# Kernel optimization log

Hardware: AMD Instinct MI355X
Metric: run time of the kernel (lower is better)

The kernel has to match this reference:

```python
import jax, jax.numpy as jnp
import numpy as np
import math

B, T, D = 2, 2048, 1024
H = 16
DH = D // H
DFF = 4096
EPS = 1e-5


def setup_inputs() -> dict:
    key = jax.random.key(0)
    ks = jax.random.split(key, 10)
    x = jax.random.normal(ks[0], (B, T, D), dtype=jnp.float32)
    # bool mask, True above diagonal => masked (matches masked_fill semantics)
    causal_mask = jnp.triu(jnp.ones((T, T), dtype=bool), k=1)
    s = 0.02
    return {
        "x": x,
        "causal_mask": causal_mask,
        "gamma1": jnp.ones((D,), jnp.float32),
        "beta1": jnp.zeros((D,), jnp.float32),
        "wq": jax.random.normal(ks[1], (D, D), jnp.float32) * s,
        "wk": jax.random.normal(ks[2], (D, D), jnp.float32) * s,
        "wv": jax.random.normal(ks[3], (D, D), jnp.float32) * s,
        "wo": jax.random.normal(ks[4], (D, D), jnp.float32) * s,
        "gamma2": jnp.ones((D,), jnp.float32),
        "beta2": jnp.zeros((D,), jnp.float32),
        "w1": jax.random.normal(ks[5], (D, DFF), jnp.float32) * s,
        "b1": jnp.zeros((DFF,), jnp.float32),
        "w2": jax.random.normal(ks[6], (DFF, D), jnp.float32) * s,
        "b2": jnp.zeros((D,), jnp.float32),
    }


def _layer_norm(x, gamma, beta):
    mean = jnp.mean(x, axis=-1, keepdims=True)
    var = jnp.mean((x - mean) ** 2, axis=-1, keepdims=True)
    xhat = (x - mean) / jnp.sqrt(var + EPS)
    return gamma * xhat + beta


def _split_heads(x):
    b, t, d = x.shape
    return x.reshape(b, t, H, DH).transpose(0, 2, 1, 3)  # (B,H,T,Dh)


def reference(x, causal_mask, gamma1, beta1, wq, wk, wv, wo,
              gamma2, beta2, w1, b1, w2, b2):
    # --- attention sublayer (pre-LN) ---
    h = _layer_norm(x, gamma1, beta1)
    q = _split_heads(h @ wq)
    k = _split_heads(h @ wk)
    v = _split_heads(h @ wv)
    scores = jnp.einsum('bhqd,bhkd->bhqk', q, k) / math.sqrt(DH)  # (B,H,T,T)
    scores = jnp.where(causal_mask[None, None, :, :], -jnp.inf, scores)
    attn = jax.nn.softmax(scores, axis=-1)
    out = jnp.einsum('bhqk,bhkd->bhqd', attn, v)
    out = out.transpose(0, 2, 1, 3).reshape(x.shape)  # merge heads
    attn_out = out @ wo
    x = x + attn_out
    # --- FFN sublayer (pre-LN) ---
    h = _layer_norm(x, gamma2, beta2)
    ffn = jax.nn.gelu(h @ w1 + b1, approximate=False) @ w2 + b2
    return x + ffn
```

## Files before the change

### kernel.cpp

```cpp
#include <hip/hip_runtime.h>
#include <hip/hip_bf16.h>
#include <math.h>

#define B_   2
#define T_   2048
#define D_   1024
#define H_   16
#define DH_  64
#define DFF_ 4096
#define NTOK (B_*T_)

typedef __attribute__((ext_vector_type(8))) short short8;
typedef __attribute__((ext_vector_type(4))) float f32x4;

static __device__ __forceinline__ short f2bf(float f) {
    union { __hip_bfloat16 h; short s; } u;
    u.h = __float2bfloat16(f);
    return u.s;
}

static __device__ __forceinline__ f32x4 mfma16(short8 a, short8 b, f32x4 c) {
    return __builtin_amdgcn_mfma_f32_16x16x32_bf16(a, b, c, 0, 0, 0);
}

static __device__ __forceinline__ void gload16(const void* g, void* l) {
    __builtin_amdgcn_global_load_lds(
        (__attribute__((address_space(1))) void*)g,
        (__attribute__((address_space(3))) void*)l, 16, 0, 0);
}

static __device__ __forceinline__ short8 lds_read_sw(const short* base, int row, int kbyte) {
    const int off = (row << 7) + (kbyte ^ ((row & 7) << 4));
    return *reinterpret_cast<const short8*>(reinterpret_cast<const char*>(base) + off);
}

__global__ __launch_bounds__(256) void transpose_cast(
    const float* __restrict__ src, short* __restrict__ dst, int K, int N, float scale)
{
    __shared__ short tile[32][33];
    const int k0 = blockIdx.y * 32, n0 = blockIdx.x * 32;
    const int tx = threadIdx.x, ty = threadIdx.y;
    #pragma unroll
    for (int j = 0; j < 4; ++j) {
        int k = ty + j * 8;
        tile[k][tx] = f2bf(src[(size_t)(k0 + k) * N + n0 + tx] * scale);
    }
    __syncthreads();
    #pragma unroll
    for (int j = 0; j < 4; ++j) {
        int n = ty + j * 8;
        dst[(size_t)(n0 + n) * K + k0 + tx] = tile[tx][n];
    }
}

__global__ __launch_bounds__(256) void ln_kernel(
    const float* __restrict__ in, const float* __restrict__ gamma,
    const float* __restrict__ beta, short* __restrict__ out)
{
    const int row = blockIdx.x;
    const int t = threadIdx.x;
    const float4 v = *reinterpret_cast<const float4*>(in + (size_t)row * D_ + t * 4);
    float s  = v.x + v.y + v.z + v.w;
    float sq = v.x*v.x + v.y*v.y + v.z*v.z + v.w*v.w;
    #pragma unroll
    for (int off = 32; off >= 1; off >>= 1) {
        s  += __shfl_xor(s, off);
        sq += __shfl_xor(sq, off);
    }
    __shared__ float ps[4], pq[4];
    if ((t & 63) == 0) { ps[t >> 6] = s; pq[t >> 6] = sq; }
    __syncthreads();
    s  = ps[0] + ps[1] + ps[2] + ps[3];
    sq = pq[0] + pq[1] + pq[2] + pq[3];
    const float mean = s * (1.0f / D_);
    float var = sq * (1.0f / D_) - mean * mean;
    var = fmaxf(var, 0.0f);
    const float rstd = rsqrtf(var + 1e-5f);
    const float4 g = *reinterpret_cast<const float4*>(gamma + t * 4);
    const float4 b = *reinterpret_cast<const float4*>(beta  + t * 4);
    short4 o;
    o.x = f2bf(g.x * ((v.x - mean) * rstd) + b.x);
    o.y = f2bf(g.y * ((v.y - mean) * rstd) + b.y);
    o.z = f2bf(g.z * ((v.z - mean) * rstd) + b.z);
    o.w = f2bf(g.w * ((v.w - mean) * rstd) + b.w);
    *reinterpret_cast<short4*>(out + (size_t)row * D_ + t * 4) = o;
}

template<int BM, int BN, int EPI>
__global__ __launch_bounds__(512) void gemm_kernel(
    const short* __restrict__ A, const short* __restrict__ Bt,
    void* __restrict__ Cout, const float* __restrict__ resid,
    const float* __restrict__ bias, short* __restrict__ vaux,
    int M, int N, int K, int nbx)
{
    constexpr int MB = BM / 4 / 16;
    constexpr int NB = BN / 2 / 16;
    constexpr int JA = BM / 64;
    constexpr int JB = BN / 64;
    constexpr int J  = JA + JB;
    __shared__ short As[2][BM * 64];
    __shared__ short Bs[2][BN * 64];
    const int t = threadIdx.x;
    const int wid = t >> 6, lane = t & 63;
    const int lr = lane & 15, lk = lane >> 4;
    const int cpx = (int)gridDim.x >> 3;
    const int bid = (int)blockIdx.x;
    const int swz = (bid & 7) * cpx + (bid >> 3);
    const int m0 = (swz / nbx) * BM, n0 = (swz % nbx) * BN;
    const int wrow = (wid >> 1) * (BM / 4);
    const int wcol = (wid & 1) * (BN / 2);

    const char* aSrc[JA];
    const char* bSrc[JB];
    #pragma unroll
    for (int j = 0; j < JA; ++j) {
        const int off = j * 8192 + t * 16;
        const int r   = off >> 7;
        const int cb  = (off & 127) ^ ((r & 7) << 4);
        aSrc[j] = (const char*)(A + (size_t)(m0 + r) * K) + cb;
    }
    #pragma unroll
    for (int j = 0; j < JB; ++j) {
        const int off = j * 8192 + t * 16;
        const int r   = off >> 7;
        const int cb  = (off & 127) ^ ((r & 7) << 4);
        bSrc[j] = (const char*)(Bt + (size_t)(n0 + r) * K) + cb;
    }

    f32x4 acc[MB][NB];
    #pragma unroll
    for (int m = 0; m < MB; ++m)
        #pragma unroll
        for (int n = 0; n < NB; ++n) acc[m][n] = (f32x4){0.f, 0.f, 0.f, 0.f};

    const int NT = K >> 6;

    auto stage = [&](int bufsel, int ktile) {
        const int kb = ktile << 7;
        #pragma unroll
        for (int j = 0; j < JA; ++j)
            gload16(aSrc[j] + kb, (char*)As[bufsel] + j * 8192 + wid * 1024);
        #pragma unroll
        for (int j = 0; j < JB; ++j)
            gload16(bSrc[j] + kb, (char*)Bs[bufsel] + j * 8192 + wid * 1024);
    };
    auto compute = [&](int bufsel) {
        #pragma unroll
        for (int kk = 0; kk < 64; kk += 32) {
            short8 af[MB], bf[NB];
            #pragma unroll
            for (int m = 0; m < MB; ++m)
                af[m] = lds_read_sw(As[bufsel], wrow + m * 16 + lr, (kk + lk * 8) * 2);
            #pragma unroll
            for (int n = 0; n < NB; ++n)
                bf[n] = lds_read_sw(Bs[bufsel], wcol + n * 16 + lr, (kk + lk * 8) * 2);
            #pragma unroll
            for (int m = 0; m < MB; ++m)
                #pragma unroll
                for (int n = 0; n < NB; ++n)
                    acc[m][n] = mfma16(af[m], bf[n], acc[m][n]);
        }
    };

    stage(0, 0);
    stage(1, 1);

    for (int kt = 0; kt < NT - 1; ++kt) {
        asm volatile("s_waitcnt vmcnt(%0)" :: "n"(J) : "memory");
        __builtin_amdgcn_s_barrier();
        compute(kt & 1);
        __builtin_amdgcn_s_barrier();
        if (kt + 2 < NT) stage(kt & 1, kt + 2);
    }
    asm volatile("s_waitcnt vmcnt(0)" ::: "memory");
    __builtin_amdgcn_s_barrier();
    compute((NT - 1) & 1);

    #pragma unroll
    for (int m = 0; m < MB; ++m) {
        #pragma unroll
        for (int n = 0; n < NB; ++n) {
            #pragma unroll
            for (int r = 0; r < 4; ++r) {
                const int gr = m0 + wrow + m * 16 + lk * 4 + r;
                const int gc = n0 + wcol + n * 16 + lr;
                const size_t idx = (size_t)gr * N + gc;
                const float v = acc[m][n][r];
                if constexpr (EPI == 0) {
                    ((short*)Cout)[idx] = f2bf(v);
                } else if constexpr (EPI == 1) {
                    ((float*)Cout)[idx] = resid[idx] + v;
                } else if constexpr (EPI == 2) {
                    const float tt = v + bias[gc];
                    const float ge = 0.5f * tt * (1.0f + erff(tt * 0.70710678118654752f));
                    ((short*)Cout)[idx] = f2bf(ge);
                } else if constexpr (EPI == 3) {
                    ((float*)Cout)[idx] = resid[idx] + v + bias[gc];
                } else {
                    if (gc < 2048) {
                        ((short*)Cout)[idx] = f2bf(v);
                    } else {
                        const int hh = (gc - 2048) >> 6, dh = (gc - 2048) & 63;
                        const int bb = gr >> 11, tl = gr & 2047;
                        vaux[((size_t)((bb << 4) + hh) * 64 + dh) * 2048 + tl] = f2bf(v);
                    }
                }
            }
        }
    }
}

static __device__ __forceinline__ void attn_tile(
    const short* Kcur, const short* Vcur, char* pw,
    short8 qf0, short8 qf1, int q0, int kvb, bool diag,
    int lr, int lk, f32x4 (&o)[4], float (&mr)[4], float (&ls)[4])
{
    f32x4 s[4];
    #pragma unroll
    for (int n = 0; n < 4; ++n) s[n] = (f32x4){0.f, 0.f, 0.f, 0.f};
    #pragma unroll
    for (int n = 0; n < 4; ++n) {
        s[n] = mfma16(qf0, lds_read_sw(Kcur, n * 16 + lr, (lk * 8) * 2), s[n]);
        s[n] = mfma16(qf1, lds_read_sw(Kcur, n * 16 + lr, (32 + lk * 8) * 2), s[n]);
    }
    #pragma unroll
    for (int r = 0; r < 4; ++r) {
        const int qg = q0 + lk * 4 + r;
        float v0 = s[0][r], v1 = s[1][r], v2 = s[2][r], v3 = s[3][r];
        if (diag) {
            if (kvb +      lr > qg) v0 = -INFINITY;
            if (kvb + 16 + lr > qg) v1 = -INFINITY;
            if (kvb + 32 + lr > qg) v2 = -INFINITY;
            if (kvb + 48 + lr > qg) v3 = -INFINITY;
        }
        const float mxl = fmaxf(fmaxf(v0, v1), fmaxf(v2, v3));
        if (!__all(mxl <= mr[r] + 8.0f)) {
            float mx = mxl;
            mx = fmaxf(mx, __shfl_xor(mx, 1));
            mx = fmaxf(mx, __shfl_xor(mx, 2));
            mx = fmaxf(mx, __shfl_xor(mx, 4));
            mx = fmaxf(mx, __shfl_xor(mx, 8));
            const float mnew = fmaxf(mr[r], mx);
            const float alpha = __builtin_amdgcn_exp2f(mr[r] - mnew);
            o[0][r] *= alpha; o[1][r] *= alpha; o[2][r] *= alpha; o[3][r] *= alpha;
            ls[r] *= alpha;
            mr[r] = mnew;
        }
        const float p0 = __builtin_amdgcn_exp2f(v0 - mr[r]);
        const float p1 = __builtin_amdgcn_exp2f(v1 - mr[r]);
        const float p2 = __builtin_amdgcn_exp2f(v2 - mr[r]);
        const float p3 = __builtin_amdgcn_exp2f(v3 - mr[r]);
        ls[r] += p0 + p1 + p2 + p3;
        const int prow = lk * 4 + r;
        const int sw = (prow & 7) << 4;
        char* prb = pw + prow * 128;
        *(short*)(prb + (((     lr * 2)) ^ sw)) = f2bf(p0);
        *(short*)(prb + ((32 + lr * 2) ^ sw)) = f2bf(p1);
        *(short*)(prb + ((64 + lr * 2) ^ sw)) = f2bf(p2);
        *(short*)(prb + ((96 + lr * 2) ^ sw)) = f2bf(p3);
    }
    asm volatile("s_waitcnt lgkmcnt(0)" ::: "memory");
    #pragma unroll
    for (int kk = 0; kk < 2; ++kk) {
        const short8 pf = *reinterpret_cast<const short8*>(
            pw + lr * 128 + ((kk * 64 + lk * 16) ^ ((lr & 7) << 4)));
        #pragma unroll
        for (int n = 0; n < 4; ++n)
            o[n] = mfma16(pf, lds_read_sw((const short*)Vcur, n * 16 + lr, (kk * 32 + lk * 8) * 2), o[n]);
    }
}

__global__ __launch_bounds__(256) void attn_kernel(
    const short* __restrict__ qkv, const short* __restrict__ vT,
    short* __restrict__ attn)
{
    __shared__ short Ks[2][4096];
    __shared__ short Vs[2][4096];
    __shared__ short Ps[2][4][1024];
    const int xx = blockIdx.x;
    const int bh = blockIdx.y;
    const int qA = xx, qB = 31 - xx;
    const int b = bh >> 4, h = bh & 15;
    const int t = threadIdx.x;
    const int wid = t >> 6, lane = t & 63;
    const int lr = lane & 15, lk = lane >> 4;
    const int q0A = qA * 64 + wid * 16;
    const int q0B = qB * 64 + wid * 16;

    const short* qrowA = qkv + (size_t)(b * T_ + q0A + lr) * 3072 + h * 64;
    const short8 qfA0 = *reinterpret_cast<const short8*>(qrowA + lk * 8);
    const short8 qfA1 = *reinterpret_cast<const short8*>(qrowA + 32 + lk * 8);
    const short* qrowB = qkv + (size_t)(b * T_ + q0B + lr) * 3072 + h * 64;
    const short8 qfB0 = *reinterpret_cast<const short8*>(qrowB + lk * 8);
    const short8 qfB1 = *reinterpret_cast<const short8*>(qrowB + 32 + lk * 8);
    const short* kbase = qkv + (size_t)b * T_ * 3072 + 1024 + h * 64;
    const short* vbase = vT + (size_t)bh * 64 * T_;

    f32x4 oA[4], oB[4];
    float mrA[4], lsA[4], mrB[4], lsB[4];
    #pragma unroll
    for (int n = 0; n < 4; ++n) {
        oA[n] = (f32x4){0.f, 0.f, 0.f, 0.f};
        oB[n] = (f32x4){0.f, 0.f, 0.f, 0.f};
    }
    #pragma unroll
    for (int r = 0; r < 4; ++r) {
        mrA[r] = -INFINITY; lsA[r] = 0.f;
        mrB[r] = -INFINITY; lsB[r] = 0.f;
    }

    const int nkt = qB + 1;

    #pragma unroll
    for (int j = 0; j < 2; ++j) {
        const int off = j * 4096 + t * 16;
        const int r   = off >> 7;
        const int cb  = (off & 127) ^ ((r & 7) << 4);
        gload16(kbase + (size_t)r * 3072 + (cb >> 1), (char*)Ks[0] + j * 4096 + wid * 1024);
        gload16(vbase + (size_t)r * T_   + (cb >> 1), (char*)Vs[0] + j * 4096 + wid * 1024);
    }
    __syncthreads();

    int cur = 0;
    for (int kt = 0; kt < nkt; ++kt) {
        const int kvb = kt * 64;
        if (kt + 1 < nkt) {
            const int nb = kvb + 64;
            #pragma unroll
            for (int j = 0; j < 2; ++j) {
                const int off = j * 4096 + t * 16;
                const int r   = off >> 7;
                const int cb  = (off & 127) ^ ((r & 7) << 4);
                gload16(kbase + (size_t)(nb + r) * 3072 + (cb >> 1),
                        (char*)Ks[cur ^ 1] + j * 4096 + wid * 1024);
                gload16(vbase + (size_t)r * T_ + nb + (cb >> 1),
                        (char*)Vs[cur ^ 1] + j * 4096 + wid * 1024);
            }
        }

        attn_tile(Ks[cur], Vs[cur], (char*)&Ps[1][wid][0],
                  qfB0, qfB1, q0B, kvb, kt == qB, lr, lk, oB, mrB, lsB);
        if (kt <= qA)
            attn_tile(Ks[cur], Vs[cur], (char*)&Ps[0][wid][0],
                      qfA0, qfA1, q0A, kvb, kt == qA, lr, lk, oA, mrA, lsA);

        __syncthreads();
        cur ^= 1;
    }

    #pragma unroll
    for (int r = 0; r < 4; ++r) {
        float lA = lsA[r], lB = lsB[r];
        lA += __shfl_xor(lA, 1); lB += __shfl_xor(lB, 1);
        lA += __shfl_xor(lA, 2); lB += __shfl_xor(lB, 2);
        lA += __shfl_xor(lA, 4); lB += __shfl_xor(lB, 4);
        lA += __shfl_xor(lA, 8); lB += __shfl_xor(lB, 8);
        const float invA = 1.0f / lA, invB = 1.0f / lB;
        short* opA = attn + (size_t)(b * T_ + q0A + lk * 4 + r) * D_ + h * 64;
        short* opB = attn + (size_t)(b * T_ + q0B + lk * 4 + r) * D_ + h * 64;
        #pragma unroll
        for (int n = 0; n < 4; ++n) {
            opA[n * 16 + lr] = f2bf(oA[n][r] * invA);
            opB[n * 16 + lr] = f2bf(oB[n][r] * invB);
        }
    }
}

extern "C" void kernel_launch(void* const* d_in, const int* in_sizes, int n_in,
                              void* d_out, int out_size, void* d_ws, size_t ws_size,
                              hipStream_t stream)
{
    (void)in_sizes; (void)n_in; (void)out_size; (void)ws_size;
    const float* x      = (const float*)d_in[0];
    const float* gamma1 = (const float*)d_in[2];
    const float* beta1  = (const float*)d_in[3];
    const float* wq     = (const float*)d_in[4];
    const float* wk     = (const float*)d_in[5];
    const float* wv     = (const float*)d_in[6];
    const float* wo     = (const float*)d_in[7];
    const float* gamma2 = (const float*)d_in[8];
    const float* beta2  = (const float*)d_in[9];
    const float* w1     = (const float*)d_in[10];
    const float* b1     = (const float*)d_in[11];
    const float* w2     = (const float*)d_in[12];
    const float* b2     = (const float*)d_in[13];
    float* out = (float*)d_out;

    char* ws = (char*)d_ws;
    size_t off = 0;
    short* wqkvT = (short*)(ws + off); off += (size_t)3072 * 1024 * 2;
    short* woT   = (short*)(ws + off); off += (size_t)1024 * 1024 * 2;
    short* w1T   = (short*)(ws + off); off += (size_t)4096 * 1024 * 2;
    short* w2T   = (short*)(ws + off); off += (size_t)1024 * 4096 * 2;
    short* h1    = (short*)(ws + off); off += (size_t)NTOK * 1024 * 2;
    short* h2    = (short*)(ws + off); off += (size_t)NTOK * 1024 * 2;
    float* y     = (float*)(ws + off); off += (size_t)NTOK * 1024 * 4;
    short* attnb = (short*)(ws + off); off += (size_t)NTOK * 1024 * 2;
    short* qkv   = (short*)(ws + off); off += (size_t)NTOK * 3072 * 2;
    short* vT    = (short*)(ws + off); off += (size_t)B_ * H_ * DH_ * T_ * 2;
    short* g     = qkv;

    const dim3 tb(32, 8);
    transpose_cast<<<dim3(32, 32),  tb, 0, stream>>>(wq, wqkvT,               1024, 1024, 0.18033688011112042f);
    transpose_cast<<<dim3(32, 32),  tb, 0, stream>>>(wk, wqkvT + 1024 * 1024, 1024, 1024, 1.0f);
    transpose_cast<<<dim3(32, 32),  tb, 0, stream>>>(wv, wqkvT + 2048 * 1024, 1024, 1024, 1.0f);
    transpose_cast<<<dim3(32, 32),  tb, 0, stream>>>(wo, woT,                 1024, 1024, 1.0f);
    transpose_cast<<<dim3(128, 32), tb, 0, stream>>>(w1, w1T, 1024, 4096, 1.0f);
    transpose_cast<<<dim3(32, 128), tb, 0, stream>>>(w2, w2T, 4096, 1024, 1.0f);

    ln_kernel<<<NTOK, 256, 0, stream>>>(x, gamma1, beta1, h1);

    gemm_kernel<128, 128, 4><<<768, 512, 0, stream>>>(
        h1, wqkvT, qkv, nullptr, nullptr, vT, NTOK, 3072, 1024, 24);

    attn_kernel<<<dim3(16, 32), 256, 0, stream>>>(qkv, vT, attnb);

    gemm_kernel<128, 64, 1><<<512, 512, 0, stream>>>(
        attnb, woT, y, x, nullptr, nullptr, NTOK, 1024, 1024, 16);

    ln_kernel<<<NTOK, 256, 0, stream>>>(y, gamma2, beta2, h2);

    gemm_kernel<128, 128, 2><<<1024, 512, 0, stream>>>(
        h2, w1T, g, nullptr, b1, nullptr, NTOK, 4096, 1024, 32);

    gemm_kernel<128, 64, 3><<<512, 512, 0, stream>>>(
        g, w2T, out, y, b2, nullptr, NTOK, 1024, 4096, 16);
}
```

Baseline: 261.0 us.

## Triple-buffer narrow GEMMs and split attention query tiles across 8 waves

Adds an NBUF template parameter to the GEMM. With three LDS buffers the next-next tile is staged right after the barrier and before compute, which removes one barrier per k-step; the two 128x64 GEMMs use this. The attention kernel now runs 512 threads: four waves handle the early query tile and four handle the late one. This replaces one set of waves processing both tiles serially, raising wave-level parallelism per block at the cost of more registers and LDS pressure per block. The early-tile waves sit idle in later iterations but still join the barriers.

```diff
diff --git a/kernel.cpp b/kernel.cpp
--- a/kernel.cpp
+++ b/kernel.cpp
@@ -86,7 +86,7 @@
     *reinterpret_cast<short4*>(out + (size_t)row * D_ + t * 4) = o;
 }
 
-template<int BM, int BN, int EPI>
+template<int BM, int BN, int EPI, int NBUF>
 __global__ __launch_bounds__(512) void gemm_kernel(
     const short* __restrict__ A, const short* __restrict__ Bt,
     void* __restrict__ Cout, const float* __restrict__ resid,
@@ -98,8 +98,8 @@
     constexpr int JA = BM / 64;
     constexpr int JB = BN / 64;
     constexpr int J  = JA + JB;
-    __shared__ short As[2][BM * 64];
-    __shared__ short Bs[2][BN * 64];
+    __shared__ short As[NBUF][BM * 64];
+    __shared__ short Bs[NBUF][BN * 64];
     const int t = threadIdx.x;
     const int wid = t >> 6, lane = t & 63;
     const int lr = lane & 15, lk = lane >> 4;
@@ -165,16 +165,28 @@
     stage(0, 0);
     stage(1, 1);
 
-    for (int kt = 0; kt < NT - 1; ++kt) {
-        asm volatile("s_waitcnt vmcnt(%0)" :: "n"(J) : "memory");
+    if constexpr (NBUF == 3) {
+        for (int kt = 0; kt < NT - 1; ++kt) {
+            asm volatile("s_waitcnt vmcnt(%0)" :: "n"(J) : "memory");
+            __builtin_amdgcn_s_barrier();
+            if (kt + 2 < NT) stage((kt + 2) % 3, kt + 2);
+            compute(kt % 3);
+        }
+        asm volatile("s_waitcnt vmcnt(0)" ::: "memory");
         __builtin_amdgcn_s_barrier();
-        compute(kt & 1);
+        compute((NT - 1) % 3);
+    } else {
+        for (int kt = 0; kt < NT - 1; ++kt) {
+            asm volatile("s_waitcnt vmcnt(%0)" :: "n"(J) : "memory");
+            __builtin_amdgcn_s_barrier();
+            compute(kt & 1);
+            __builtin_amdgcn_s_barrier();
+            if (kt + 2 < NT) stage(kt & 1, kt + 2);
+        }
+        asm volatile("s_waitcnt vmcnt(0)" ::: "memory");
         __builtin_amdgcn_s_barrier();
-        if (kt + 2 < NT) stage(kt & 1, kt + 2);
-    }
-    asm volatile("s_waitcnt vmcnt(0)" ::: "memory");
-    __builtin_amdgcn_s_barrier();
-    compute((NT - 1) & 1);
+        compute((NT - 1) & 1);
+    }
 
     #pragma unroll
     for (int m = 0; m < MB; ++m) {
@@ -270,54 +282,43 @@
     }
 }
 
-__global__ __launch_bounds__(256) void attn_kernel(
+__global__ __launch_bounds__(512) void attn_kernel(
     const short* __restrict__ qkv, const short* __restrict__ vT,
     short* __restrict__ attn)
 {
     __shared__ short Ks[2][4096];
     __shared__ short Vs[2][4096];
-    __shared__ short Ps[2][4][1024];
+    __shared__ short Ps[8][1024];
     const int xx = blockIdx.x;
     const int bh = blockIdx.y;
-    const int qA = xx, qB = 31 - xx;
     const int b = bh >> 4, h = bh & 15;
     const int t = threadIdx.x;
     const int wid = t >> 6, lane = t & 63;
     const int lr = lane & 15, lk = lane >> 4;
-    const int q0A = qA * 64 + wid * 16;
-    const int q0B = qB * 64 + wid * 16;
-
-    const short* qrowA = qkv + (size_t)(b * T_ + q0A + lr) * 3072 + h * 64;
-    const short8 qfA0 = *reinterpret_cast<const short8*>(qrowA + lk * 8);
-    const short8 qfA1 = *reinterpret_cast<const short8*>(qrowA + 32 + lk * 8);
-    const short* qrowB = qkv + (size_t)(b * T_ + q0B + lr) * 3072 + h * 64;
-    const short8 qfB0 = *reinterpret_cast<const short8*>(qrowB + lk * 8);
-    const short8 qfB1 = *reinterpret_cast<const short8*>(qrowB + 32 + lk * 8);
+    const int qt = (wid < 4) ? xx : 31 - xx;
+    const int q0 = qt * 64 + (wid & 3) * 16;
+
+    const short* qrow = qkv + (size_t)(b * T_ + q0 + lr) * 3072 + h * 64;
+    const short8 qf0 = *reinterpret_cast<const short8*>(qrow + lk * 8);
+    const short8 qf1 = *reinterpret_cast<const short8*>(qrow + 32 + lk * 8);
     const short* kbase = qkv + (size_t)b * T_ * 3072 + 1024 + h * 64;
     const short* vbase = vT + (size_t)bh * 64 * T_;
 
-    f32x4 oA[4], oB[4];
-    float mrA[4], lsA[4], mrB[4], lsB[4];
-    #pragma unroll
-    for (int n = 0; n < 4; ++n) {
-        oA[n] = (f32x4){0.f, 0.f, 0.f, 0.f};
-        oB[n] = (f32x4){0.f, 0.f, 0.f, 0.f};
-    }
-    #pragma unroll
-    for (int r = 0; r < 4; ++r) {
-        mrA[r] = -INFINITY; lsA[r] = 0.f;
-        mrB[r] = -INFINITY; lsB[r] = 0.f;
-    }
-
-    const int nkt = qB + 1;
-
-    #pragma unroll
-    for (int j = 0; j < 2; ++j) {
-        const int off = j * 4096 + t * 16;
+    f32x4 o[4];
+    float mr[4], ls[4];
+    #pragma unroll
+    for (int n = 0; n < 4; ++n) o[n] = (f32x4){0.f, 0.f, 0.f, 0.f};
+    #pragma unroll
+    for (int r = 0; r < 4; ++r) { mr[r] = -INFINITY; ls[r] = 0.f; }
+
+    const int nkt = 32 - xx;
+
+    {
+        const int off = t * 16;
         const int r   = off >> 7;
         const int cb  = (off & 127) ^ ((r & 7) << 4);
-        gload16(kbase + (size_t)r * 3072 + (cb >> 1), (char*)Ks[0] + j * 4096 + wid * 1024);
-        gload16(vbase + (size_t)r * T_   + (cb >> 1), (char*)Vs[0] + j * 4096 + wid * 1024);
+        gload16(kbase + (size_t)r * 3072 + (cb >> 1), (char*)Ks[0] + wid * 1024);
+        gload16(vbase + (size_t)r * T_   + (cb >> 1), (char*)Vs[0] + wid * 1024);
     }
     __syncthreads();
 
@@ -326,23 +327,18 @@
         const int kvb = kt * 64;
         if (kt + 1 < nkt) {
             const int nb = kvb + 64;
-            #pragma unroll
-            for (int j = 0; j < 2; ++j) {
-                const int off = j * 4096 + t * 16;
-                const int r   = off >> 7;
-                const int cb  = (off & 127) ^ ((r & 7) << 4);
-                gload16(kbase + (size_t)(nb + r) * 3072 + (cb >> 1),
-                        (char*)Ks[cur ^ 1] + j * 4096 + wid * 1024);
-                gload16(vbase + (size_t)r * T_ + nb + (cb >> 1),
-                        (char*)Vs[cur ^ 1] + j * 4096 + wid * 1024);
-            }
-        }
-
-        attn_tile(Ks[cur], Vs[cur], (char*)&Ps[1][wid][0],
-                  qfB0, qfB1, q0B, kvb, kt == qB, lr, lk, oB, mrB, lsB);
-        if (kt <= qA)
-            attn_tile(Ks[cur], Vs[cur], (char*)&Ps[0][wid][0],
-                      qfA0, qfA1, q0A, kvb, kt == qA, lr, lk, oA, mrA, lsA);
+            const int off = t * 16;
+            const int r   = off >> 7;
+            const int cb  = (off & 127) ^ ((r & 7) << 4);
+            gload16(kbase + (size_t)(nb + r) * 3072 + (cb >> 1),
+                    (char*)Ks[cur ^ 1] + wid * 1024);
+            gload16(vbase + (size_t)r * T_ + nb + (cb >> 1),
+                    (char*)Vs[cur ^ 1] + wid * 1024);
+        }
+
+        if (kt <= qt)
+            attn_tile(Ks[cur], Vs[cur], (char*)&Ps[wid][0],
+                      qf0, qf1, q0, kvb, kt == qt, lr, lk, o, mr, ls);
 
         __syncthreads();
         cur ^= 1;
@@ -350,19 +346,16 @@
 
     #pragma unroll
     for (int r = 0; r < 4; ++r) {
-        float lA = lsA[r], lB = lsB[r];
-        lA += __shfl_xor(lA, 1); lB += __shfl_xor(lB, 1);
-        lA += __shfl_xor(lA, 2); lB += __shfl_xor(lB, 2);
-        lA += __shfl_xor(lA, 4); lB += __shfl_xor(lB, 4);
-        lA += __shfl_xor(lA, 8); lB += __shfl_xor(lB, 8);
-        const float invA = 1.0f / lA, invB = 1.0f / lB;
-        short* opA = attn + (size_t)(b * T_ + q0A + lk * 4 + r) * D_ + h * 64;
-        short* opB = attn + (size_t)(b * T_ + q0B + lk * 4 + r) * D_ + h * 64;
-        #pragma unroll
-        for (int n = 0; n < 4; ++n) {
-            opA[n * 16 + lr] = f2bf(oA[n][r] * invA);
-            opB[n * 16 + lr] = f2bf(oB[n][r] * invB);
-        }
+        float l = ls[r];
+        l += __shfl_xor(l, 1);
+        l += __shfl_xor(l, 2);
+        l += __shfl_xor(l, 4);
+        l += __shfl_xor(l, 8);
+        const float inv = 1.0f / l;
+        short* op = attn + (size_t)(b * T_ + q0 + lk * 4 + r) * D_ + h * 64;
+        #pragma unroll
+        for (int n = 0; n < 4; ++n)
+            op[n * 16 + lr] = f2bf(o[n][r] * inv);
     }
 }
 
@@ -410,19 +403,19 @@
 
     ln_kernel<<<NTOK, 256, 0, stream>>>(x, gamma1, beta1, h1);
 
-    gemm_kernel<128, 128, 4><<<768, 512, 0, stream>>>(
+    gemm_kernel<128, 128, 4, 2><<<768, 512, 0, stream>>>(
         h1, wqkvT, qkv, nullptr, nullptr, vT, NTOK, 3072, 1024, 24);
 
-    attn_kernel<<<dim3(16, 32), 256, 0, stream>>>(qkv, vT, attnb);
-
-    gemm_kernel<128, 64, 1><<<512, 512, 0, stream>>>(
+    attn_kernel<<<dim3(16, 32), 512, 0, stream>>>(qkv, vT, attnb);
+
+    gemm_kernel<128, 64, 1, 3><<<512, 512, 0, stream>>>(
         attnb, woT, y, x, nullptr, nullptr, NTOK, 1024, 1024, 16);
 
     ln_kernel<<<NTOK, 256, 0, stream>>>(y, gamma2, beta2, h2);
 
-    gemm_kernel<128, 128, 2><<<1024, 512, 0, stream>>>(
+    gemm_kernel<128, 128, 2, 2><<<1024, 512, 0, stream>>>(
         h2, w1T, g, nullptr, b1, nullptr, NTOK, 4096, 1024, 32);
 
-    gemm_kernel<128, 64, 3><<<512, 512, 0, stream>>>(
+    gemm_kernel<128, 64, 3, 3><<<512, 512, 0, stream>>>(
         g, w2T, out, y, b2, nullptr, NTOK, 1024, 4096, 16);
 }
```

Measured after the change: 289.4 us. 10.9% more time.
